# Kernel tuning notes

Measured on AMD Instinct MI355X. Metric: run time of the kernel, lower is better.

The kernel has to match this reference:

```python
import jax, jax.numpy as jnp
import numpy as np

N = 100000      # nodes
E = 800000      # edges
D_IN = 128
H = 4           # heads
C = 32          # out channels per head (out_feature = H*C = 128)
EPS = 1e-5


def setup_inputs() -> dict:
    key = jax.random.key(0)
    ks = jax.random.split(key, 12)
    x = jax.random.normal(ks[0], (N, D_IN), dtype=jnp.float32)
    edge_index = jax.random.randint(ks[1], (2, E), 0, N, dtype=jnp.int32)
    edge_weights = jax.random.uniform(ks[2], (E, 1), dtype=jnp.float32)
    s = 1.0 / np.sqrt(D_IN)
    W_l = jax.random.uniform(ks[3], (D_IN, H * C), jnp.float32, -s, s)   # GATv2 lin_l (source)
    W_r = jax.random.uniform(ks[4], (D_IN, H * C), jnp.float32, -s, s)   # GATv2 lin_r (target)
    W_e = jax.random.uniform(ks[5], (1, H * C), jnp.float32, -1.0, 1.0)  # lin_edge (edge_dim=1)
    att = jax.random.uniform(ks[6], (H, C), jnp.float32, -s, s)          # attention vector
    bias = jnp.zeros((H * C,), jnp.float32)
    gamma = jnp.ones((H * C,), jnp.float32)   # BatchNorm weight
    beta = jnp.zeros((H * C,), jnp.float32)   # BatchNorm bias
    return {"x": x, "edge_index": edge_index, "edge_weights": edge_weights,
            "W_l": W_l, "W_r": W_r, "W_e": W_e, "att": att, "bias": bias,
            "gamma": gamma, "beta": beta}


def reference(x, edge_index, edge_weights, W_l, W_r, W_e, att, bias, gamma, beta):
    src = edge_index[0]  # message source j
    dst = edge_index[1]  # message target i (aggregation index)

    x_l = (x @ W_l).reshape(N, H, C)
    x_r = (x @ W_r).reshape(N, H, C)
    e = (edge_weights @ W_e).reshape(E, H, C)

    # GATv2 message: LeakyReLU(x_j + x_i + e, 0.2), score = <att, .>
    xj = x_l[src]                                  # [E,H,C]
    m = jax.nn.leaky_relu(xj + x_r[dst] + e, 0.2)  # [E,H,C]
    logits = jnp.einsum('ehc,hc->eh', m, att)      # [E,H]

    # segment softmax over edges sharing the same destination
    seg_max = jax.ops.segment_max(logits, dst, num_segments=N)  # [N,H]
    seg_max = jnp.where(jnp.isfinite(seg_max), seg_max, 0.0)
    expv = jnp.exp(logits - seg_max[dst])
    seg_sum = jax.ops.segment_sum(expv, dst, num_segments=N)
    alpha = expv / (seg_sum[dst] + 1e-16)          # [E,H]

    out = jax.ops.segment_sum(xj * alpha[:, :, None], dst, num_segments=N)  # [N,H,C]
    out = out.reshape(N, H * C) + bias

    # BatchNorm1d over nodes (training-mode batch statistics, biased var)
    mu = jnp.mean(out, axis=0)
    var = jnp.var(out, axis=0)
    out = gamma * (out - mu) * jax.lax.rsqrt(var + EPS) + beta

    # F.leaky_relu default negative_slope=0.01; dropout is identity in eval
    return jax.nn.leaky_relu(out, 0.01)
```

## Files before the change

kernel.cpp:

```cpp
#include <hip/hip_runtime.h>

#define D 128
#define HEADS 4

typedef __bf16 v8bf __attribute__((ext_vector_type(8)));
typedef float v4f __attribute__((ext_vector_type(4)));

__device__ __forceinline__ unsigned short f2bfbits(float f) {
    unsigned u = __float_as_uint(f);
    u += 0x7FFFu + ((u >> 16) & 1u);
    return (unsigned short)(u >> 16);
}

__device__ __forceinline__ float4 ldbf4(const __bf16* p) {
    const uint2 u = *reinterpret_cast<const uint2*>(p);
    float4 r;
    r.x = __uint_as_float(u.x << 16);
    r.y = __uint_as_float(u.x & 0xFFFF0000u);
    r.z = __uint_as_float(u.y << 16);
    r.w = __uint_as_float(u.y & 0xFFFF0000u);
    return r;
}

__global__ __launch_bounds__(256) void deg_wprep_k(
    const int* __restrict__ dst, int* __restrict__ deg, int E,
    const float* __restrict__ Wl, const float* __restrict__ Wr,
    __bf16* __restrict__ Wbf, int degBlocks) {
    if ((int)blockIdx.x < degBlocks) {
        const int e = blockIdx.x * 256 + threadIdx.x;
        if (e < E) atomicAdd(&deg[dst[e]], 1);
        return;
    }
    const int i = ((int)blockIdx.x - degBlocks) * 256 + threadIdx.x;
    const int cg = i >> 7;
    const int k = i & 127;
    const float* __restrict__ Wp = (cg < D) ? Wl : Wr;
    Wbf[i] = (__bf16)Wp[(size_t)k * D + (cg & (D - 1))];
}

__global__ __launch_bounds__(256) void scan1_k(
    const int* __restrict__ deg, int* __restrict__ rowptr,
    int* __restrict__ bsum, int n) {
    __shared__ int tmp[256];
    const int i = blockIdx.x * 256 + threadIdx.x;
    const int v = (i < n) ? deg[i] : 0;
    tmp[threadIdx.x] = v;
    __syncthreads();
    for (int off = 1; off < 256; off <<= 1) {
        int t = (threadIdx.x >= off) ? tmp[threadIdx.x - off] : 0;
        __syncthreads();
        tmp[threadIdx.x] += t;
        __syncthreads();
    }
    if (i < n) rowptr[i] = tmp[threadIdx.x] - v;
    if (threadIdx.x == 255) bsum[blockIdx.x] = tmp[255];
}

__global__ __launch_bounds__(256) void scan3_k(
    int* __restrict__ rowptr, const int* __restrict__ bsum,
    int* __restrict__ cursor, int n, int E) {
    __shared__ int wsum[4];
    int acc = 0;
    for (int j = threadIdx.x; j < blockIdx.x; j += 256) acc += bsum[j];
#pragma unroll
    for (int off = 1; off < 64; off <<= 1) acc += __shfl_xor(acc, off);
    if ((threadIdx.x & 63) == 0) wsum[threadIdx.x >> 6] = acc;
    __syncthreads();
    const int prefix = wsum[0] + wsum[1] + wsum[2] + wsum[3];
    const int i = blockIdx.x * 256 + threadIdx.x;
    if (i < n) {
        const int r = rowptr[i] + prefix;
        rowptr[i] = r;
        cursor[i] = r;
    } else if (i == n) {
        rowptr[n] = E;
    }
}

__global__ __launch_bounds__(256) void gemm_fill_k(
    const float* __restrict__ x, const __bf16* __restrict__ Wbf,
    __bf16* __restrict__ xl, __bf16* __restrict__ xr, int n,
    const int* __restrict__ src, const int* __restrict__ dst,
    const float* __restrict__ ew, int* __restrict__ cursor,
    int2* __restrict__ epay, int E, int gemmBlocks) {
    if ((int)blockIdx.x >= gemmBlocks) {
        const int f = (int)blockIdx.x - gemmBlocks;
        const int xcd = f & 7;
        const int nchunk = ((int)gridDim.x - gemmBlocks) >> 3;
        const int slice = (n + 7) >> 3;
        const int lo = xcd * slice;
        const int hi = min(n, lo + slice);
        const int stride = nchunk * 256;
        for (int e = (f >> 3) * 256 + threadIdx.x; e < E; e += stride) {
            const int d = dst[e];
            if (d >= lo && d < hi) {
                const int p = atomicAdd(&cursor[d], 1);
                int2 v;
                v.x = src[e];
                v.y = __float_as_int(ew[e]);
                epay[p] = v;
            }
        }
        return;
    }
    __shared__ __align__(16) unsigned short xs[64][136];
    const int tid = threadIdx.x;
    const int row0 = blockIdx.x * 64;
    const int lane = tid & 63;
    const int wid = tid >> 6;
    const int col16 = lane & 15;
    const int kg = lane >> 4;

    for (int i = tid; i < 1024; i += 256) {
        const int r = i >> 4;
        const int k0 = (i & 15) * 8;
        const int row = row0 + r;
        float4 v0 = make_float4(0.f, 0.f, 0.f, 0.f), v1 = v0;
        if (row < n) {
            v0 = *reinterpret_cast<const float4*>(&x[(size_t)row * D + k0]);
            v1 = *reinterpret_cast<const float4*>(&x[(size_t)row * D + k0 + 4]);
        }
        uint4 p;
        p.x = ((unsigned)f2bfbits(v0.y) << 16) | f2bfbits(v0.x);
        p.y = ((unsigned)f2bfbits(v0.w) << 16) | f2bfbits(v0.z);
        p.z = ((unsigned)f2bfbits(v1.y) << 16) | f2bfbits(v1.x);
        p.w = ((unsigned)f2bfbits(v1.w) << 16) | f2bfbits(v1.z);
        *reinterpret_cast<uint4*>(&xs[r][k0]) = p;
    }

    v8bf bfr[4][4];
#pragma unroll
    for (int nt = 0; nt < 4; ++nt) {
        const int cg = (wid * 4 + nt) * 16 + col16;
#pragma unroll
        for (int ks = 0; ks < 4; ++ks)
            bfr[nt][ks] = *reinterpret_cast<const v8bf*>(
                &Wbf[(size_t)cg * 128 + ks * 32 + kg * 8]);
    }
    __syncthreads();

    v4f acc[4][4] = {};
#pragma unroll
    for (int mt = 0; mt < 4; ++mt) {
        v8bf afr[4];
#pragma unroll
        for (int ks = 0; ks < 4; ++ks)
            afr[ks] = *reinterpret_cast<const v8bf*>(&xs[mt * 16 + col16][ks * 32 + kg * 8]);
#pragma unroll
        for (int nt = 0; nt < 4; ++nt)
#pragma unroll
            for (int ks = 0; ks < 4; ++ks)
                acc[mt][nt] = __builtin_amdgcn_mfma_f32_16x16x32_bf16(
                    afr[ks], bfr[nt][ks], acc[mt][nt], 0, 0, 0);
    }

#pragma unroll
    for (int mt = 0; mt < 4; ++mt)
#pragma unroll
        for (int nt = 0; nt < 4; ++nt) {
            const int cg = (wid * 4 + nt) * 16 + col16;
            __bf16* __restrict__ op = (cg < D) ? xl : xr;
            const int c = cg & (D - 1);
#pragma unroll
            for (int r = 0; r < 4; ++r) {
                const int row = row0 + mt * 16 + kg * 4 + r;
                if (row < n) op[(size_t)row * D + c] = (__bf16)acc[mt][nt][r];
            }
        }
}

__global__ __launch_bounds__(256) void node_aggr_k(
    const __bf16* __restrict__ xl, const __bf16* __restrict__ xr,
    const int2* __restrict__ epay, const int* __restrict__ rowptr,
    const float* __restrict__ We, const float* __restrict__ att,
    __bf16* __restrict__ outb, int n) {
    const int wgl = (int)((blockIdx.x * (size_t)blockDim.x + threadIdx.x) >> 6);
    const int lane = threadIdx.x & 63;
    const int half = lane >> 5;
    const int node = wgl * 2 + half;
    const int ch = (lane & 31) * 4;

    int beg = 0, end = 0;
    if (node < n) {
        beg = rowptr[node];
        end = rowptr[node + 1];
    }
    const int dg = end - beg;
    const int tmax = max(dg, __shfl_xor(dg, 32));

    float4 b = make_float4(0.f, 0.f, 0.f, 0.f);
    if (node < n) b = ldbf4(&xr[(size_t)node * D + ch]);
    const float4 we4 = *reinterpret_cast<const float4*>(&We[ch]);
    const float4 at4 = *reinterpret_cast<const float4*>(&att[ch]);

    float s = 0.f;
    float4 acc = make_float4(0.f, 0.f, 0.f, 0.f);
    for (int t = 0; t < tmax; t += 2) {
        float part[2];
        float4 av[2];
#pragma unroll
        for (int i = 0; i < 2; ++i) {
            const int p = beg + t + i;
            const int q = max(min(p, end - 1), 0);
            const int2 pw = epay[q];
            av[i] = ldbf4(&xl[(size_t)pw.x * D + ch]);
            const float wgt = __int_as_float(pw.y);
            float c0 = fmaf(wgt, we4.x, av[i].x + b.x);
            float c1 = fmaf(wgt, we4.y, av[i].y + b.y);
            float c2 = fmaf(wgt, we4.z, av[i].z + b.z);
            float c3 = fmaf(wgt, we4.w, av[i].w + b.w);
            c0 = fmaxf(c0, 0.2f * c0);
            c1 = fmaxf(c1, 0.2f * c1);
            c2 = fmaxf(c2, 0.2f * c2);
            c3 = fmaxf(c3, 0.2f * c3);
            part[i] = fmaf(c3, at4.w, fmaf(c2, at4.z, fmaf(c1, at4.y, c0 * at4.x)));
        }
#pragma unroll
        for (int off = 1; off < 8; off <<= 1) {
            part[0] += __shfl_xor(part[0], off);
            part[1] += __shfl_xor(part[1], off);
        }
        const float pv0 = (t + 0 < dg) ? __expf(fminf(part[0], 50.f)) : 0.f;
        const float pv1 = (t + 1 < dg) ? __expf(fminf(part[1], 50.f)) : 0.f;
        s += pv0 + pv1;
        acc.x += fmaf(pv1, av[1].x, pv0 * av[0].x);
        acc.y += fmaf(pv1, av[1].y, pv0 * av[0].y);
        acc.z += fmaf(pv1, av[1].z, pv0 * av[0].z);
        acc.w += fmaf(pv1, av[1].w, pv0 * av[0].w);
    }
    if (node < n) {
        const float inv = 1.f / (s + 1e-16f);
        uint2 pkt;
        pkt.x = ((unsigned)f2bfbits(acc.y * inv) << 16) | f2bfbits(acc.x * inv);
        pkt.y = ((unsigned)f2bfbits(acc.w * inv) << 16) | f2bfbits(acc.z * inv);
        *reinterpret_cast<uint2*>(&outb[(size_t)node * D + ch]) = pkt;
    }
}

__global__ __launch_bounds__(256) void bn_partial_k(
    const __bf16* __restrict__ outb, float* __restrict__ sums,
    float* __restrict__ sumsq, int n) {
    __shared__ float rs[8][128];
    __shared__ float rq[8][128];
    const int c4 = (threadIdx.x & 31) * 4;
    const int rstr = threadIdx.x >> 5;
    float4 s = make_float4(0.f, 0.f, 0.f, 0.f);
    float4 q = make_float4(0.f, 0.f, 0.f, 0.f);
    for (int r = blockIdx.x * 8 + rstr; r < n; r += gridDim.x * 8) {
        const float4 v = ldbf4(&outb[(size_t)r * D + c4]);
        s.x += v.x; s.y += v.y; s.z += v.z; s.w += v.w;
        q.x = fmaf(v.x, v.x, q.x);
        q.y = fmaf(v.y, v.y, q.y);
        q.z = fmaf(v.z, v.z, q.z);
        q.w = fmaf(v.w, v.w, q.w);
    }
    rs[rstr][c4 + 0] = s.x; rs[rstr][c4 + 1] = s.y;
    rs[rstr][c4 + 2] = s.z; rs[rstr][c4 + 3] = s.w;
    rq[rstr][c4 + 0] = q.x; rq[rstr][c4 + 1] = q.y;
    rq[rstr][c4 + 2] = q.z; rq[rstr][c4 + 3] = q.w;
    __syncthreads();
    const int t = threadIdx.x;
    if (t < 128) {
        float a = 0.f;
#pragma unroll
        for (int j = 0; j < 8; ++j) a += rs[j][t];
        atomicAdd(&sums[t], a);
    } else {
        const int c = t - 128;
        float a = 0.f;
#pragma unroll
        for (int j = 0; j < 8; ++j) a += rq[j][c];
        atomicAdd(&sumsq[c], a);
    }
}

__global__ __launch_bounds__(256) void bn_apply_k(
    const __bf16* __restrict__ outb, float* __restrict__ out,
    const float* __restrict__ bnsums, const float* __restrict__ gamma,
    const float* __restrict__ beta, int n, int total4) {
    const int i = blockIdx.x * blockDim.x + threadIdx.x;
    if (i >= total4) return;
    const int c4 = (i & 31) * 4;
    const float inv_n = 1.f / (float)n;
    const float4 sm = *reinterpret_cast<const float4*>(&bnsums[c4]);
    const float4 sq = *reinterpret_cast<const float4*>(&bnsums[D + c4]);
    const float4 g = *reinterpret_cast<const float4*>(&gamma[c4]);
    const float4 bt = *reinterpret_cast<const float4*>(&beta[c4]);
    float4 v = ldbf4(&outb[(size_t)i * 4]);
    float mu, var, scale, shift, r;
    mu = sm.x * inv_n; var = fmaxf(sq.x * inv_n - mu * mu, 0.f);
    scale = g.x * rsqrtf(var + 1e-5f); shift = bt.x - mu * scale;
    r = fmaf(v.x, scale, shift); v.x = fmaxf(r, 0.01f * r);
    mu = sm.y * inv_n; var = fmaxf(sq.y * inv_n - mu * mu, 0.f);
    scale = g.y * rsqrtf(var + 1e-5f); shift = bt.y - mu * scale;
    r = fmaf(v.y, scale, shift); v.y = fmaxf(r, 0.01f * r);
    mu = sm.z * inv_n; var = fmaxf(sq.z * inv_n - mu * mu, 0.f);
    scale = g.z * rsqrtf(var + 1e-5f); shift = bt.z - mu * scale;
    r = fmaf(v.z, scale, shift); v.z = fmaxf(r, 0.01f * r);
    mu = sm.w * inv_n; var = fmaxf(sq.w * inv_n - mu * mu, 0.f);
    scale = g.w * rsqrtf(var + 1e-5f); shift = bt.w - mu * scale;
    r = fmaf(v.w, scale, shift); v.w = fmaxf(r, 0.01f * r);
    *reinterpret_cast<float4*>(&out[(size_t)i * 4]) = v;
}

extern "C" void kernel_launch(void* const* d_in, const int* in_sizes, int n_in,
                              void* d_out, int out_size, void* d_ws, size_t ws_size,
                              hipStream_t stream) {
    const float* x     = (const float*)d_in[0];
    const int*   ei    = (const int*)d_in[1];
    const float* ew    = (const float*)d_in[2];
    const float* Wl    = (const float*)d_in[3];
    const float* Wr    = (const float*)d_in[4];
    const float* We    = (const float*)d_in[5];
    const float* att   = (const float*)d_in[6];
    const float* gamma = (const float*)d_in[8];
    const float* beta  = (const float*)d_in[9];

    const int n = in_sizes[0] / D;
    const int E = in_sizes[2];
    const int* src = ei;
    const int* dst = ei + E;
    const int nblk = (n + 255) / 256;

    char* ws = (char*)d_ws;
    size_t off = 0;
    __bf16* xl = (__bf16*)(ws + off);   off += (size_t)n * D * 2;
    __bf16* xr = (__bf16*)(ws + off);   off += (size_t)n * D * 2;
    __bf16* outb = (__bf16*)(ws + off); off += (size_t)n * D * 2;
    __bf16* Wbf = (__bf16*)(ws + off);  off += (size_t)2 * D * D * 2;
    float* bnsums = (float*)(ws + off); off += 2 * D * sizeof(float);
    int* deg = (int*)(ws + off);        off += (size_t)n * sizeof(int);
    int* rowptr = (int*)(ws + off);     off += ((size_t)n + 1) * sizeof(int);
    int* cursor = (int*)(ws + off);     off += (size_t)n * sizeof(int);
    int* bsum = (int*)(ws + off);       off += (size_t)nblk * sizeof(int);
    off = (off + 15) & ~(size_t)15;
    int2* epay = (int2*)(ws + off);     off += (size_t)E * sizeof(int2);

    float* outacc = (float*)d_out;

    hipMemsetAsync(bnsums, 0, (2 * D + (size_t)n) * sizeof(float), stream);

    const int degBlocks = (E + 255) / 256;
    deg_wprep_k<<<degBlocks + 128, 256, 0, stream>>>(dst, deg, E, Wl, Wr, Wbf,
                                                     degBlocks);

    scan1_k<<<nblk, 256, 0, stream>>>(deg, rowptr, bsum, n);
    scan3_k<<<nblk + 1, 256, 0, stream>>>(rowptr, bsum, cursor, n, E);

    const int gemmBlocks = (n + 63) / 64;
    gemm_fill_k<<<gemmBlocks + 2048, 256, 0, stream>>>(
        x, Wbf, xl, xr, n, src, dst, ew, cursor, epay, E, gemmBlocks);

    const int waves = (n + 1) / 2;
    node_aggr_k<<<(waves + 3) / 4, 256, 0, stream>>>(xl, xr, epay, rowptr,
                                                     We, att, outb, n);

    bn_partial_k<<<512, 256, 0, stream>>>(outb, bnsums, bnsums + D, n);
    bn_apply_k<<<((n * D / 4) + 255) / 256, 256, 0, stream>>>(
        outb, outacc, bnsums, gamma, beta, n, n * D / 4);
}
```

Before: 196.5 us.

## Spread GEMM blocks across degree, scan and fill kernels to overlap work

The node projection GEMM, which used to run as one kernel paired with the fill step, is now split into four chunks. Each chunk is appended as extra blocks to the degree-count, scan1, scan3 and fill kernels, so the short, latency-bound scan kernels share the GPU with useful MFMA work. Weight conversion gets its own small kernel ahead of these. The x-to-bf16 conversion now uses a native cast instead of manual rounding bits. A kernel that contains a gemm_body path needs the larger shared-memory footprint, which may reduce occupancy for the scan and fill blocks.

Measured after the change: 207.0 us. 1.05x slower.

```diff
diff --git a/kernel.cpp b/kernel.cpp
--- a/kernel.cpp
+++ b/kernel.cpp
@@ -1,7 +1,6 @@
 #include <hip/hip_runtime.h>
 
 #define D 128
-#define HEADS 4
 
 typedef __bf16 v8bf __attribute__((ext_vector_type(8)));
 typedef float v4f __attribute__((ext_vector_type(4)));
@@ -22,25 +21,112 @@
     return r;
 }
 
-__global__ __launch_bounds__(256) void deg_wprep_k(
-    const int* __restrict__ dst, int* __restrict__ deg, int E,
+__device__ __forceinline__ void gemm_body(
+    int gb, const float* __restrict__ x, const __bf16* __restrict__ Wbf,
+    __bf16* __restrict__ xl, __bf16* __restrict__ xr, int n) {
+    __shared__ __align__(16) unsigned short xs[64][136];
+    const int tid = threadIdx.x;
+    const int row0 = gb * 64;
+    const int lane = tid & 63;
+    const int wid = tid >> 6;
+    const int col16 = lane & 15;
+    const int kg = lane >> 4;
+
+    for (int i = tid; i < 1024; i += 256) {
+        const int r = i >> 4;
+        const int k0 = (i & 15) * 8;
+        const int row = row0 + r;
+        float4 v0 = make_float4(0.f, 0.f, 0.f, 0.f), v1 = v0;
+        if (row < n) {
+            v0 = *reinterpret_cast<const float4*>(&x[(size_t)row * D + k0]);
+            v1 = *reinterpret_cast<const float4*>(&x[(size_t)row * D + k0 + 4]);
+        }
+        v8bf t;
+        t[0] = (__bf16)v0.x; t[1] = (__bf16)v0.y;
+        t[2] = (__bf16)v0.z; t[3] = (__bf16)v0.w;
+        t[4] = (__bf16)v1.x; t[5] = (__bf16)v1.y;
+        t[6] = (__bf16)v1.z; t[7] = (__bf16)v1.w;
+        *reinterpret_cast<v8bf*>(&xs[r][k0]) = t;
+    }
+
+    v8bf bfr[4][4];
+#pragma unroll
+    for (int nt = 0; nt < 4; ++nt) {
+        const int cg = (wid * 4 + nt) * 16 + col16;
+#pragma unroll
+        for (int ks = 0; ks < 4; ++ks)
+            bfr[nt][ks] = *reinterpret_cast<const v8bf*>(
+                &Wbf[(size_t)cg * 128 + ks * 32 + kg * 8]);
+    }
+    __syncthreads();
+
+    v4f acc[4][4] = {};
+#pragma unroll
+    for (int mt = 0; mt < 4; ++mt) {
+        v8bf afr[4];
+#pragma unroll
+        for (int ks = 0; ks < 4; ++ks)
+            afr[ks] = *reinterpret_cast<const v8bf*>(&xs[mt * 16 + col16][ks * 32 + kg * 8]);
+#pragma unroll
+        for (int nt = 0; nt < 4; ++nt)
+#pragma unroll
+            for (int ks = 0; ks < 4; ++ks)
+                acc[mt][nt] = __builtin_amdgcn_mfma_f32_16x16x32_bf16(
+                    afr[ks], bfr[nt][ks], acc[mt][nt], 0, 0, 0);
+    }
+
+#pragma unroll
+    for (int mt = 0; mt < 4; ++mt)
+#pragma unroll
+        for (int nt = 0; nt < 4; ++nt) {
+            const int cg = (wid * 4 + nt) * 16 + col16;
+            __bf16* __restrict__ op = (cg < D) ? xl : xr;
+            const int c = cg & (D - 1);
+#pragma unroll
+            for (int r = 0; r < 4; ++r) {
+                const int row = row0 + mt * 16 + kg * 4 + r;
+                if (row < n) op[(size_t)row * D + c] = (__bf16)acc[mt][nt][r];
+            }
+        }
+}
+
+__global__ __launch_bounds__(256) void wprep_k(
     const float* __restrict__ Wl, const float* __restrict__ Wr,
-    __bf16* __restrict__ Wbf, int degBlocks) {
-    if ((int)blockIdx.x < degBlocks) {
-        const int e = blockIdx.x * 256 + threadIdx.x;
-        if (e < E) atomicAdd(&deg[dst[e]], 1);
-        return;
-    }
-    const int i = ((int)blockIdx.x - degBlocks) * 256 + threadIdx.x;
+    __bf16* __restrict__ Wbf) {
+    const int i = blockIdx.x * 256 + threadIdx.x;
     const int cg = i >> 7;
     const int k = i & 127;
     const float* __restrict__ Wp = (cg < D) ? Wl : Wr;
     Wbf[i] = (__bf16)Wp[(size_t)k * D + (cg & (D - 1))];
 }
 
-__global__ __launch_bounds__(256) void scan1_k(
+__global__ __launch_bounds__(256) void deg_gemm_k(
+    const int* __restrict__ dst, int* __restrict__ deg, int E, int frontBlocks,
+    const float* __restrict__ x, const __bf16* __restrict__ Wbf,
+    __bf16* __restrict__ xl, __bf16* __restrict__ xr, int n,
+    int gemmBase, int gemmBlocks) {
+    const int fb = (int)blockIdx.x - frontBlocks;
+    if (fb < 0) {
+        const int e = blockIdx.x * 256 + threadIdx.x;
+        if (e < E) atomicAdd(&deg[dst[e]], 1);
+        return;
+    }
+    const int gb = gemmBase + fb;
+    if (gb < gemmBlocks) gemm_body(gb, x, Wbf, xl, xr, n);
+}
+
+__global__ __launch_bounds__(256) void scan1_gemm_k(
     const int* __restrict__ deg, int* __restrict__ rowptr,
-    int* __restrict__ bsum, int n) {
+    int* __restrict__ bsum, int n, int frontBlocks,
+    const float* __restrict__ x, const __bf16* __restrict__ Wbf,
+    __bf16* __restrict__ xl, __bf16* __restrict__ xr,
+    int gemmBase, int gemmBlocks) {
+    const int fb = (int)blockIdx.x - frontBlocks;
+    if (fb >= 0) {
+        const int gb = gemmBase + fb;
+        if (gb < gemmBlocks) gemm_body(gb, x, Wbf, xl, xr, n);
+        return;
+    }
     __shared__ int tmp[256];
     const int i = blockIdx.x * 256 + threadIdx.x;
     const int v = (i < n) ? deg[i] : 0;
@@ -56,9 +142,18 @@
     if (threadIdx.x == 255) bsum[blockIdx.x] = tmp[255];
 }
 
-__global__ __launch_bounds__(256) void scan3_k(
+__global__ __launch_bounds__(256) void scan3_gemm_k(
     int* __restrict__ rowptr, const int* __restrict__ bsum,
-    int* __restrict__ cursor, int n, int E) {
+    int* __restrict__ cursor, int n, int E, int frontBlocks,
+    const float* __restrict__ x, const __bf16* __restrict__ Wbf,
+    __bf16* __restrict__ xl, __bf16* __restrict__ xr,
+    int gemmBase, int gemmBlocks) {
+    const int fb = (int)blockIdx.x - frontBlocks;
+    if (fb >= 0) {
+        const int gb = gemmBase + fb;
+        if (gb < gemmBlocks) gemm_body(gb, x, Wbf, xl, xr, n);
+        return;
+    }
     __shared__ int wsum[4];
     int acc = 0;
     for (int j = threadIdx.x; j < blockIdx.x; j += 256) acc += bsum[j];
@@ -77,96 +172,36 @@
     }
 }
 
-__global__ __launch_bounds__(256) void gemm_fill_k(
-    const float* __restrict__ x, const __bf16* __restrict__ Wbf,
-    __bf16* __restrict__ xl, __bf16* __restrict__ xr, int n,
+__global__ __launch_bounds__(256) void fill_gemm_k(
     const int* __restrict__ src, const int* __restrict__ dst,
     const float* __restrict__ ew, int* __restrict__ cursor,
-    int2* __restrict__ epay, int E, int gemmBlocks) {
-    if ((int)blockIdx.x >= gemmBlocks) {
-        const int f = (int)blockIdx.x - gemmBlocks;
-        const int xcd = f & 7;
-        const int nchunk = ((int)gridDim.x - gemmBlocks) >> 3;
-        const int slice = (n + 7) >> 3;
-        const int lo = xcd * slice;
-        const int hi = min(n, lo + slice);
-        const int stride = nchunk * 256;
-        for (int e = (f >> 3) * 256 + threadIdx.x; e < E; e += stride) {
-            const int d = dst[e];
-            if (d >= lo && d < hi) {
-                const int p = atomicAdd(&cursor[d], 1);
-                int2 v;
-                v.x = src[e];
-                v.y = __float_as_int(ew[e]);
-                epay[p] = v;
-            }
+    int2* __restrict__ epay, int E, int n, int frontBlocks,
+    const float* __restrict__ x, const __bf16* __restrict__ Wbf,
+    __bf16* __restrict__ xl, __bf16* __restrict__ xr,
+    int gemmBase, int gemmBlocks) {
+    const int fb = (int)blockIdx.x - frontBlocks;
+    if (fb >= 0) {
+        const int gb = gemmBase + fb;
+        if (gb < gemmBlocks) gemm_body(gb, x, Wbf, xl, xr, n);
+        return;
+    }
+    const int f = (int)blockIdx.x;
+    const int xcd = f & 7;
+    const int nchunk = frontBlocks >> 3;
+    const int slice = (n + 7) >> 3;
+    const int lo = xcd * slice;
+    const int hi = min(n, lo + slice);
+    const int stride = nchunk * 256;
+    for (int e = (f >> 3) * 256 + threadIdx.x; e < E; e += stride) {
+        const int d = dst[e];
+        if (d >= lo && d < hi) {
+            const int p = atomicAdd(&cursor[d], 1);
+            int2 v;
+            v.x = src[e];
+            v.y = __float_as_int(ew[e]);
+            epay[p] = v;
         }
-        return;
-    }
-    __shared__ __align__(16) unsigned short xs[64][136];
-    const int tid = threadIdx.x;
-    const int row0 = blockIdx.x * 64;
-    const int lane = tid & 63;
-    const int wid = tid >> 6;
-    const int col16 = lane & 15;
-    const int kg = lane >> 4;
-
-    for (int i = tid; i < 1024; i += 256) {
-        const int r = i >> 4;
-        const int k0 = (i & 15) * 8;
-        const int row = row0 + r;
-        float4 v0 = make_float4(0.f, 0.f, 0.f, 0.f), v1 = v0;
-        if (row < n) {
-            v0 = *reinterpret_cast<const float4*>(&x[(size_t)row * D + k0]);
-            v1 = *reinterpret_cast<const float4*>(&x[(size_t)row * D + k0 + 4]);
-        }
-        uint4 p;
-        p.x = ((unsigned)f2bfbits(v0.y) << 16) | f2bfbits(v0.x);
-        p.y = ((unsigned)f2bfbits(v0.w) << 16) | f2bfbits(v0.z);
-        p.z = ((unsigned)f2bfbits(v1.y) << 16) | f2bfbits(v1.x);
-        p.w = ((unsigned)f2bfbits(v1.w) << 16) | f2bfbits(v1.z);
-        *reinterpret_cast<uint4*>(&xs[r][k0]) = p;
-    }
-
-    v8bf bfr[4][4];
-#pragma unroll
-    for (int nt = 0; nt < 4; ++nt) {
-        const int cg = (wid * 4 + nt) * 16 + col16;
-#pragma unroll
-        for (int ks = 0; ks < 4; ++ks)
-            bfr[nt][ks] = *reinterpret_cast<const v8bf*>(
-                &Wbf[(size_t)cg * 128 + ks * 32 + kg * 8]);
-    }
-    __syncthreads();
-
-    v4f acc[4][4] = {};
-#pragma unroll
-    for (int mt = 0; mt < 4; ++mt) {
-        v8bf afr[4];
-#pragma unroll
-        for (int ks = 0; ks < 4; ++ks)
-            afr[ks] = *reinterpret_cast<const v8bf*>(&xs[mt * 16 + col16][ks * 32 + kg * 8]);
-#pragma unroll
-        for (int nt = 0; nt < 4; ++nt)
-#pragma unroll
-            for (int ks = 0; ks < 4; ++ks)
-                acc[mt][nt] = __builtin_amdgcn_mfma_f32_16x16x32_bf16(
-                    afr[ks], bfr[nt][ks], acc[mt][nt], 0, 0, 0);
-    }
-
-#pragma unroll
-    for (int mt = 0; mt < 4; ++mt)
-#pragma unroll
-        for (int nt = 0; nt < 4; ++nt) {
-            const int cg = (wid * 4 + nt) * 16 + col16;
-            __bf16* __restrict__ op = (cg < D) ? xl : xr;
-            const int c = cg & (D - 1);
-#pragma unroll
-            for (int r = 0; r < 4; ++r) {
-                const int row = row0 + mt * 16 + kg * 4 + r;
-                if (row < n) op[(size_t)row * D + c] = (__bf16)acc[mt][nt][r];
-            }
-        }
+    }
 }
 
 __global__ __launch_bounds__(256) void node_aggr_k(
@@ -340,16 +375,26 @@
 
     hipMemsetAsync(bnsums, 0, (2 * D + (size_t)n) * sizeof(float), stream);
 
+    const int gemmBlocks = (n + 63) / 64;
     const int degBlocks = (E + 255) / 256;
-    deg_wprep_k<<<degBlocks + 128, 256, 0, stream>>>(dst, deg, E, Wl, Wr, Wbf,
-                                                     degBlocks);
-
-    scan1_k<<<nblk, 256, 0, stream>>>(deg, rowptr, bsum, n);
-    scan3_k<<<nblk + 1, 256, 0, stream>>>(rowptr, bsum, cursor, n, E);
-
-    const int gemmBlocks = (n + 63) / 64;
-    gemm_fill_k<<<gemmBlocks + 2048, 256, 0, stream>>>(
-        x, Wbf, xl, xr, n, src, dst, ew, cursor, epay, E, gemmBlocks);
+    const int fillBlocks = 2048;
+    const int g1 = 512, g2 = 256, g3 = 256;
+    const int g4 = gemmBlocks - g1 - g2 - g3;
+
+    wprep_k<<<128, 256, 0, stream>>>(Wl, Wr, Wbf);
+
+    deg_gemm_k<<<degBlocks + g1, 256, 0, stream>>>(
+        dst, deg, E, degBlocks, x, Wbf, xl, xr, n, 0, gemmBlocks);
+
+    scan1_gemm_k<<<nblk + g2, 256, 0, stream>>>(
+        deg, rowptr, bsum, n, nblk, x, Wbf, xl, xr, g1, gemmBlocks);
+
+    scan3_gemm_k<<<(nblk + 1) + g3, 256, 0, stream>>>(
+        rowptr, bsum, cursor, n, E, nblk + 1, x, Wbf, xl, xr, g1 + g2, gemmBlocks);
+
+    fill_gemm_k<<<fillBlocks + g4, 256, 0, stream>>>(
+        src, dst, ew, cursor, epay, E, n, fillBlocks, x, Wbf, xl, xr,
+        g1 + g2 + g3, gemmBlocks);
 
     const int waves = (n + 1) / 2;
     node_aggr_k<<<(waves + 3) / 4, 256, 0, stream>>>(xl, xr, epay, rowptr,
```

## Split GEMM into persistent prefetching kernel and separate CSR fill kernel

Applied to the files above, without the earlier changes.

Moves the x@[W_l|W_r] GEMM out of the combined gemm/fill kernel into a persistent 512-block kernel. Each block loads the weight fragments into registers once and prefetches the next tile of x into registers while the MFMAs on the current tile run. The GEMM now launches right after the weight prep, before the scan kernels, and the CSR edge fill becomes its own kernel. This saves the per-tile weight reloads and hides global load latency, at the cost of no longer overlapping the GEMM with the atomic fill inside one launch, and of fewer resident blocks.

Result: no change. 198.8 us (+1.2%).

```diff
diff --git a/kernel.cpp b/kernel.cpp
--- a/kernel.cpp
+++ b/kernel.cpp
@@ -1,7 +1,6 @@
 #include <hip/hip_runtime.h>
 
 #define D 128
-#define HEADS 4
 
 typedef __bf16 v8bf __attribute__((ext_vector_type(8)));
 typedef float v4f __attribute__((ext_vector_type(4)));
@@ -36,6 +35,113 @@
     const int k = i & 127;
     const float* __restrict__ Wp = (cg < D) ? Wl : Wr;
     Wbf[i] = (__bf16)Wp[(size_t)k * D + (cg & (D - 1))];
+}
+
+__global__ __launch_bounds__(256, 1) void gemm_persist_k(
+    const float* __restrict__ x, const __bf16* __restrict__ Wbf,
+    __bf16* __restrict__ xl, __bf16* __restrict__ xr, int n, int nTiles) {
+    __shared__ __align__(16) unsigned short xs[64][136];
+    const int tid = threadIdx.x;
+    const int lane = tid & 63;
+    const int wid = tid >> 6;
+    const int col16 = lane & 15;
+    const int kg = lane >> 4;
+
+    v8bf bfr[4][4];
+#pragma unroll
+    for (int nt = 0; nt < 4; ++nt) {
+        const int cg = (wid * 4 + nt) * 16 + col16;
+#pragma unroll
+        for (int ks = 0; ks < 4; ++ks)
+            bfr[nt][ks] = *reinterpret_cast<const v8bf*>(
+                &Wbf[(size_t)cg * 128 + ks * 32 + kg * 8]);
+    }
+
+    v8bf pre[4];
+    int tile = (int)blockIdx.x;
+    {
+        const int row0 = tile * 64;
+#pragma unroll
+        for (int j = 0; j < 4; ++j) {
+            const int i = tid + j * 256;
+            const int row = row0 + (i >> 4);
+            const int k0 = (i & 15) * 8;
+            float4 v0 = make_float4(0.f, 0.f, 0.f, 0.f), v1 = v0;
+            if (row < n) {
+                v0 = *reinterpret_cast<const float4*>(&x[(size_t)row * D + k0]);
+                v1 = *reinterpret_cast<const float4*>(&x[(size_t)row * D + k0 + 4]);
+            }
+            v8bf t;
+            t[0] = (__bf16)v0.x; t[1] = (__bf16)v0.y;
+            t[2] = (__bf16)v0.z; t[3] = (__bf16)v0.w;
+            t[4] = (__bf16)v1.x; t[5] = (__bf16)v1.y;
+            t[6] = (__bf16)v1.z; t[7] = (__bf16)v1.w;
+            pre[j] = t;
+        }
+    }
+
+    while (tile < nTiles) {
+        const int row0 = tile * 64;
+#pragma unroll
+        for (int j = 0; j < 4; ++j) {
+            const int i = tid + j * 256;
+            *reinterpret_cast<v8bf*>(&xs[i >> 4][(i & 15) * 8]) = pre[j];
+        }
+        __syncthreads();
+
+        const int next = tile + (int)gridDim.x;
+        if (next < nTiles) {
+            const int nrow0 = next * 64;
+#pragma unroll
+            for (int j = 0; j < 4; ++j) {
+                const int i = tid + j * 256;
+                const int row = nrow0 + (i >> 4);
+                const int k0 = (i & 15) * 8;
+                float4 v0 = make_float4(0.f, 0.f, 0.f, 0.f), v1 = v0;
+                if (row < n) {
+                    v0 = *reinterpret_cast<const float4*>(&x[(size_t)row * D + k0]);
+                    v1 = *reinterpret_cast<const float4*>(&x[(size_t)row * D + k0 + 4]);
+                }
+                v8bf t;
+                t[0] = (__bf16)v0.x; t[1] = (__bf16)v0.y;
+                t[2] = (__bf16)v0.z; t[3] = (__bf16)v0.w;
+                t[4] = (__bf16)v1.x; t[5] = (__bf16)v1.y;
+                t[6] = (__bf16)v1.z; t[7] = (__bf16)v1.w;
+                pre[j] = t;
+            }
+        }
+
+        v4f acc[4][4] = {};
+#pragma unroll
+        for (int mt = 0; mt < 4; ++mt) {
+            v8bf afr[4];
+#pragma unroll
+            for (int ks = 0; ks < 4; ++ks)
+                afr[ks] = *reinterpret_cast<const v8bf*>(
+                    &xs[mt * 16 + col16][ks * 32 + kg * 8]);
+#pragma unroll
+            for (int nt = 0; nt < 4; ++nt)
+#pragma unroll
+                for (int ks = 0; ks < 4; ++ks)
+                    acc[mt][nt] = __builtin_amdgcn_mfma_f32_16x16x32_bf16(
+                        afr[ks], bfr[nt][ks], acc[mt][nt], 0, 0, 0);
+        }
+#pragma unroll
+        for (int mt = 0; mt < 4; ++mt)
+#pragma unroll
+            for (int nt = 0; nt < 4; ++nt) {
+                const int cg = (wid * 4 + nt) * 16 + col16;
+                __bf16* __restrict__ op = (cg < D) ? xl : xr;
+                const int c = cg & (D - 1);
+#pragma unroll
+                for (int r = 0; r < 4; ++r) {
+                    const int row = row0 + mt * 16 + kg * 4 + r;
+                    if (row < n) op[(size_t)row * D + c] = (__bf16)acc[mt][nt][r];
+                }
+            }
+        __syncthreads();
+        tile = next;
+    }
 }
 
 __global__ __launch_bounds__(256) void scan1_k(
@@ -77,96 +183,26 @@
     }
 }
 
-__global__ __launch_bounds__(256) void gemm_fill_k(
-    const float* __restrict__ x, const __bf16* __restrict__ Wbf,
-    __bf16* __restrict__ xl, __bf16* __restrict__ xr, int n,
+__global__ __launch_bounds__(256) void fill_k(
     const int* __restrict__ src, const int* __restrict__ dst,
     const float* __restrict__ ew, int* __restrict__ cursor,
-    int2* __restrict__ epay, int E, int gemmBlocks) {
-    if ((int)blockIdx.x >= gemmBlocks) {
-        const int f = (int)blockIdx.x - gemmBlocks;
-        const int xcd = f & 7;
-        const int nchunk = ((int)gridDim.x - gemmBlocks) >> 3;
-        const int slice = (n + 7) >> 3;
-        const int lo = xcd * slice;
-        const int hi = min(n, lo + slice);
-        const int stride = nchunk * 256;
-        for (int e = (f >> 3) * 256 + threadIdx.x; e < E; e += stride) {
-            const int d = dst[e];
-            if (d >= lo && d < hi) {
-                const int p = atomicAdd(&cursor[d], 1);
-                int2 v;
-                v.x = src[e];
-                v.y = __float_as_int(ew[e]);
-                epay[p] = v;
-            }
-        }
-        return;
-    }
-    __shared__ __align__(16) unsigned short xs[64][136];
-    const int tid = threadIdx.x;
-    const int row0 = blockIdx.x * 64;
-    const int lane = tid & 63;
-    const int wid = tid >> 6;
-    const int col16 = lane & 15;
-    const int kg = lane >> 4;
-
-    for (int i = tid; i < 1024; i += 256) {
-        const int r = i >> 4;
-        const int k0 = (i & 15) * 8;
-        const int row = row0 + r;
-        float4 v0 = make_float4(0.f, 0.f, 0.f, 0.f), v1 = v0;
-        if (row < n) {
-            v0 = *reinterpret_cast<const float4*>(&x[(size_t)row * D + k0]);
-            v1 = *reinterpret_cast<const float4*>(&x[(size_t)row * D + k0 + 4]);
-        }
-        uint4 p;
-        p.x = ((unsigned)f2bfbits(v0.y) << 16) | f2bfbits(v0.x);
-        p.y = ((unsigned)f2bfbits(v0.w) << 16) | f2bfbits(v0.z);
-        p.z = ((unsigned)f2bfbits(v1.y) << 16) | f2bfbits(v1.x);
-        p.w = ((unsigned)f2bfbits(v1.w) << 16) | f2bfbits(v1.z);
-        *reinterpret_cast<uint4*>(&xs[r][k0]) = p;
-    }
-
-    v8bf bfr[4][4];
-#pragma unroll
-    for (int nt = 0; nt < 4; ++nt) {
-        const int cg = (wid * 4 + nt) * 16 + col16;
-#pragma unroll
-        for (int ks = 0; ks < 4; ++ks)
-            bfr[nt][ks] = *reinterpret_cast<const v8bf*>(
-                &Wbf[(size_t)cg * 128 + ks * 32 + kg * 8]);
-    }
-    __syncthreads();
-
-    v4f acc[4][4] = {};
-#pragma unroll
-    for (int mt = 0; mt < 4; ++mt) {
-        v8bf afr[4];
-#pragma unroll
-        for (int ks = 0; ks < 4; ++ks)
-            afr[ks] = *reinterpret_cast<const v8bf*>(&xs[mt * 16 + col16][ks * 32 + kg * 8]);
-#pragma unroll
-        for (int nt = 0; nt < 4; ++nt)
-#pragma unroll
-            for (int ks = 0; ks < 4; ++ks)
-                acc[mt][nt] = __builtin_amdgcn_mfma_f32_16x16x32_bf16(
-                    afr[ks], bfr[nt][ks], acc[mt][nt], 0, 0, 0);
-    }
-
-#pragma unroll
-    for (int mt = 0; mt < 4; ++mt)
-#pragma unroll
-        for (int nt = 0; nt < 4; ++nt) {
-            const int cg = (wid * 4 + nt) * 16 + col16;
-            __bf16* __restrict__ op = (cg < D) ? xl : xr;
-            const int c = cg & (D - 1);
-#pragma unroll
-            for (int r = 0; r < 4; ++r) {
-                const int row = row0 + mt * 16 + kg * 4 + r;
-                if (row < n) op[(size_t)row * D + c] = (__bf16)acc[mt][nt][r];
-            }
-        }
+    int2* __restrict__ epay, int E, int n) {
+    const int xcd = blockIdx.x & 7;
+    const int nchunk = gridDim.x >> 3;
+    const int slice = (n + 7) >> 3;
+    const int lo = xcd * slice;
+    const int hi = min(n, lo + slice);
+    const int stride = nchunk * 256;
+    for (int e = ((int)blockIdx.x >> 3) * 256 + threadIdx.x; e < E; e += stride) {
+        const int d = dst[e];
+        if (d >= lo && d < hi) {
+            const int p = atomicAdd(&cursor[d], 1);
+            int2 v;
+            v.x = src[e];
+            v.y = __float_as_int(ew[e]);
+            epay[p] = v;
+        }
+    }
 }
 
 __global__ __launch_bounds__(256) void node_aggr_k(
@@ -344,12 +380,13 @@
     deg_wprep_k<<<degBlocks + 128, 256, 0, stream>>>(dst, deg, E, Wl, Wr, Wbf,
                                                      degBlocks);
 
+    const int nTiles = (n + 63) / 64;
+    gemm_persist_k<<<512, 256, 0, stream>>>(x, Wbf, xl, xr, n, nTiles);
+
     scan1_k<<<nblk, 256, 0, stream>>>(deg, rowptr, bsum, n);
     scan3_k<<<nblk + 1, 256, 0, stream>>>(rowptr, bsum, cursor, n, E);
 
-    const int gemmBlocks = (n + 63) / 64;
-    gemm_fill_k<<<gemmBlocks + 2048, 256, 0, stream>>>(
-        x, Wbf, xl, xr, n, src, dst, ew, cursor, epay, E, gemmBlocks);
+    fill_k<<<2048, 256, 0, stream>>>(src, dst, ew, cursor, epay, E, n);
 
     const int waves = (n + 1) / 2;
     node_aggr_k<<<(waves + 3) / 4, 256, 0, stream>>>(xl, xr, epay, rowptr,
```
